# Performance work log

Measured on AMD Instinct MI355X. Metric: run time of the kernel, lower is better.

Reference implementation:

```python
import jax, jax.numpy as jnp
import numpy as np
from math import sqrt

B, S, D_MODEL, H, DK, DV = 16, 512, 256, 8, 32, 32
EPS = 1e-5


def layer_norm(x, g, b):
    m = jnp.mean(x, axis=-1, keepdims=True)
    v = jnp.mean((x - m) ** 2, axis=-1, keepdims=True)
    return g * (x - m) / jnp.sqrt(v + EPS) + b


def setup_inputs() -> dict:
    key = jax.random.key(0)
    ks = jax.random.split(key, 16)
    inp = {
        "input_Q": jax.random.normal(ks[0], (B, S, D_MODEL), jnp.float32),
        "input_K": jax.random.normal(ks[1], (B, S, D_MODEL), jnp.float32),
        "input_V": jax.random.normal(ks[2], (B, S, D_MODEL), jnp.float32),
        "attn_mask": jax.random.bernoulli(ks[3], 0.1, (B, H, S, S)),
        "matrix": jax.random.uniform(ks[4], (B, S, S), jnp.float32),
        # learned params (stored [in, out], i.e. transpose of torch Linear weight)
        "W_Q": jax.random.normal(ks[5], (D_MODEL, H * DK), jnp.float32) * 0.02,
        "W_K": jax.random.normal(ks[6], (D_MODEL, H * DK), jnp.float32) * 0.02,
        "W_V": jax.random.normal(ks[7], (D_MODEL, H * DV), jnp.float32) * 0.02,
        "W_V2": jax.random.normal(ks[8], (D_MODEL, DV), jnp.float32) * 0.02,
        "W_fc": jax.random.normal(ks[9], (DV * (H + 1), D_MODEL), jnp.float32) * 0.02,
        "ln_g": jnp.ones((D_MODEL,), jnp.float32),
        "ln_b": jnp.zeros((D_MODEL,), jnp.float32),
        "fu_ln_g": jnp.ones((H + 1,), jnp.float32),
        "fu_ln_b": jnp.zeros((H + 1,), jnp.float32),
        "fu_w1": jax.random.normal(ks[10], (H + 1, 6), jnp.float32) * 0.3,
        "fu_b1": jnp.zeros((6,), jnp.float32),
        "fu_w2": jax.random.normal(ks[11], (6, 1), jnp.float32) * 0.3,
        "fu_b2": jnp.zeros((1,), jnp.float32),
    }
    return inp


def reference(input_Q, input_K, input_V, attn_mask, matrix,
              W_Q, W_K, W_V, W_V2, W_fc, ln_g, ln_b,
              fu_ln_g, fu_ln_b, fu_w1, fu_b1, fu_w2, fu_b2):
    b = input_Q.shape[0]
    # project and split heads: [B, H, S, d]
    Q = (input_Q @ W_Q).reshape(b, -1, H, DK).transpose(0, 2, 1, 3)
    K = (input_K @ W_K).reshape(b, -1, H, DK).transpose(0, 2, 1, 3)
    V = (input_V @ W_V).reshape(b, -1, H, DV).transpose(0, 2, 1, 3)
    scores = jnp.einsum('bhqd,bhkd->bhqk', Q, K) / sqrt(DK)
    scores = jnp.where(attn_mask, -1e9, scores)
    attn = jax.nn.softmax(scores, axis=-1)            # [B, H, S, S]
    context = jnp.einsum('bhqk,bhkd->bhqd', attn, V)  # [B, H, S, DV]
    # second context from pairwise matrix
    context2 = matrix @ (input_V @ W_V2)              # [B, S, DV]
    # gated matrix update: concat matrix with attn maps along head axis
    gate_in = jnp.concatenate([matrix[:, None], attn], axis=1)  # [B, H+1, S, S]
    gate_in = gate_in.transpose(0, 3, 2, 1)                     # [B, S, S, H+1]
    g = layer_norm(gate_in, fu_ln_g, fu_ln_b)
    g = jax.nn.relu(g @ fu_w1 + fu_b1)
    g = jax.nn.sigmoid(g @ fu_w2 + fu_b2)[..., 0]               # [B, S, S]
    matrix_out = matrix * g
    # merge heads, concat, project, layernorm
    context = context.transpose(0, 2, 1, 3).reshape(b, -1, H * DV)
    context = jnp.concatenate([context, context2], axis=-1)     # [B, S, DV*(H+1)]
    output = layer_norm(context @ W_fc, ln_g, ln_b)
    return (output, matrix_out)
```

## Files before the change

### kernel.cpp

```cpp
#include <hip/hip_runtime.h>
#include <hip/hip_bf16.h>

#define BB 16
#define SS 512
#define DM 256
#define NH 8

#define OFF_QB    0
#define OFF_KB    1048576
#define OFF_VT    2097152
#define OFF_VP2   3145728
#define OFF_CTXB  3407872
#define OFF_CTX2B 4456448
#define OFF_G     4587520
#define OFF_FLAG  6684672
#define OFF_PM    6684674

#define SCALE 0.17677669529663687f
#define KE2 0.2550348623f

typedef __attribute__((ext_vector_type(8))) short bfrag8;
typedef __attribute__((ext_vector_type(4))) float facc4;

__global__ void mask_or_kernel(const unsigned int* __restrict__ w,
                               unsigned int* __restrict__ acc) {
  __shared__ unsigned int sh[256];
  unsigned int a = 0;
  int base = blockIdx.x * 1024;
  for (int i = threadIdx.x; i < 1024; i += 256) a |= w[base + i];
  sh[threadIdx.x] = a;
  __syncthreads();
  for (int s = 128; s > 0; s >>= 1) {
    if (threadIdx.x < s) sh[threadIdx.x] |= sh[threadIdx.x + s];
    __syncthreads();
  }
  if (threadIdx.x == 0) atomicOr(acc, sh[0]);
}

__global__ __launch_bounds__(256) void mask_pack_kernel(
    const void* __restrict__ mask, unsigned long long* __restrict__ pm,
    const unsigned int* __restrict__ orv) {
  const unsigned int rawor = *orv;
  const int flagv = (rawor <= 1u) ? 0 : ((rawor == 0x3F800000u) ? 2 : 1);
  const int lane = threadIdx.x & 63;
  const int wv = threadIdx.x >> 6;
  const int w0 = (blockIdx.x * 4 + wv) * 32;
  const unsigned char* mb = (const unsigned char*)mask;
  const int* mi = (const int*)mask;
  const float* mf = (const float*)mask;
  unsigned long long myw = 0;
#pragma unroll 4
  for (int i = 0; i < 32; i++) {
    long long idx = (long long)(w0 + i) * 64 + lane;
    bool m;
    if (flagv == 1) m = (mb[idx] != 0);
    else if (flagv == 0) m = (mi[idx] != 0);
    else m = (mf[idx] != 0.f);
    unsigned long long bits = __ballot(m);
    if (lane == i) myw = bits;
  }
  if (lane < 32) pm[w0 + lane] = myw;
}

__global__ __launch_bounds__(256) void gemm_qkv_kernel(
    const float* __restrict__ inQ, const float* __restrict__ inK,
    const float* __restrict__ inV,
    const float* __restrict__ Wq, const float* __restrict__ Wk,
    const float* __restrict__ Wv,
    __hip_bfloat16* __restrict__ Qb, __hip_bfloat16* __restrict__ Kb,
    __hip_bfloat16* __restrict__ Vt) {
  __shared__ __align__(16) __hip_bfloat16 As[64][40];
  __shared__ __align__(16) __hip_bfloat16 Bs[64][40];
  const int tid = threadIdx.x;
  const int bid = blockIdx.x;
  const int matid = bid >> 9;
  const int mblk = (bid & 511) >> 2;
  const int nblk = bid & 3;
  const int m0 = mblk * 64;
  const int n0 = nblk * 64;
  const float* X = (matid == 0) ? inQ : (matid == 1) ? inK : inV;
  const float* W = (matid == 0) ? Wq : (matid == 1) ? Wk : Wv;

  const int lane = tid & 63;
  const int w = tid >> 6;
  const int wm = w & 1, wn = w >> 1;
  const int cl = lane & 15, quad = lane >> 4;
  const int arow = tid >> 2, ak8 = (tid & 3) * 8;
  const int bn = tid & 63, bk8 = (tid >> 6) * 8;

  facc4 acc[2][2];
#pragma unroll
  for (int t = 0; t < 2; t++)
#pragma unroll
    for (int u = 0; u < 2; u++) acc[t][u] = (facc4){0.f, 0.f, 0.f, 0.f};

#pragma unroll 1
  for (int kc = 0; kc < 8; kc++) {
    float4 x0 = *(const float4*)&X[(m0 + arow) * 256 + kc * 32 + ak8];
    float4 x1 = *(const float4*)&X[(m0 + arow) * 256 + kc * 32 + ak8 + 4];
    float wv[8];
#pragma unroll
    for (int j = 0; j < 8; j++) wv[j] = W[(kc * 32 + bk8 + j) * 256 + n0 + bn];
    __syncthreads();
    {
      __hip_bfloat16 ta[8];
      ta[0] = __float2bfloat16(x0.x); ta[1] = __float2bfloat16(x0.y);
      ta[2] = __float2bfloat16(x0.z); ta[3] = __float2bfloat16(x0.w);
      ta[4] = __float2bfloat16(x1.x); ta[5] = __float2bfloat16(x1.y);
      ta[6] = __float2bfloat16(x1.z); ta[7] = __float2bfloat16(x1.w);
      *(uint4*)&As[arow][ak8] = *(uint4*)ta;
      __hip_bfloat16 tb[8];
#pragma unroll
      for (int j = 0; j < 8; j++) tb[j] = __float2bfloat16(wv[j]);
      *(uint4*)&Bs[bn][bk8] = *(uint4*)tb;
    }
    __syncthreads();
    bfrag8 aA[2], bB[2];
#pragma unroll
    for (int t = 0; t < 2; t++)
      aA[t] = *(const bfrag8*)&As[wm * 32 + t * 16 + cl][quad * 8];
#pragma unroll
    for (int u = 0; u < 2; u++)
      bB[u] = *(const bfrag8*)&Bs[wn * 32 + u * 16 + cl][quad * 8];
#pragma unroll
    for (int t = 0; t < 2; t++)
#pragma unroll
      for (int u = 0; u < 2; u++)
        acc[t][u] =
            __builtin_amdgcn_mfma_f32_16x16x32_bf16(aA[t], bB[u], acc[t][u], 0, 0, 0);
  }

  if (matid < 2) {
    __hip_bfloat16* Y = (matid == 0) ? Qb : Kb;
#pragma unroll
    for (int t = 0; t < 2; t++)
#pragma unroll
      for (int u = 0; u < 2; u++)
#pragma unroll
        for (int reg = 0; reg < 4; reg++)
          Y[(m0 + wm * 32 + t * 16 + quad * 4 + reg) * 256 + n0 + wn * 32 +
            u * 16 + cl] = __float2bfloat16(acc[t][u][reg]);
  } else {
#pragma unroll
    for (int t = 0; t < 2; t++)
#pragma unroll
      for (int u = 0; u < 2; u++) {
        int c = n0 + wn * 32 + u * 16 + cl;
        int mg = m0 + wm * 32 + t * 16 + quad * 4;
        int b = mg >> 9, s = mg & 511;
        __hip_bfloat16 pk[4];
#pragma unroll
        for (int reg = 0; reg < 4; reg++)
          pk[reg] = __float2bfloat16(acc[t][u][reg]);
        *(ushort4*)&Vt[(((b << 8) + c) << 9) + s] = *(ushort4*)pk;
      }
  }
}

__global__ __launch_bounds__(256) void vp2_kernel(
    const float* __restrict__ inV, const float* __restrict__ Wv2,
    float* __restrict__ Vp2) {
  __shared__ __align__(16) float xs[16][260];
  const int t = threadIdx.x;
  const int r0 = blockIdx.x * 16;
  for (int e = t; e < 16 * 256; e += 256) {
    int r = e >> 8, i = e & 255;
    xs[r][i] = inV[(r0 + r) * 256 + i];
  }
  __syncthreads();
  const int c2 = t & 31, rr = t >> 5;
  float a0 = 0.f, a1 = 0.f;
  for (int i = 0; i < 256; i += 4) {
    float w0 = Wv2[i * 32 + c2], w1 = Wv2[(i + 1) * 32 + c2];
    float w2 = Wv2[(i + 2) * 32 + c2], w3 = Wv2[(i + 3) * 32 + c2];
    float4 xa = *(const float4*)&xs[rr][i];
    float4 xb = *(const float4*)&xs[rr + 8][i];
    a0 += xa.x * w0 + xa.y * w1 + xa.z * w2 + xa.w * w3;
    a1 += xb.x * w0 + xb.y * w1 + xb.z * w2 + xb.w * w3;
  }
  Vp2[(r0 + rr) * 32 + c2] = a0;
  Vp2[(r0 + rr + 8) * 32 + c2] = a1;
}

__global__ __launch_bounds__(512, 2) void attn_kernel(
    const __hip_bfloat16* __restrict__ Qb, const __hip_bfloat16* __restrict__ Kb,
    const __hip_bfloat16* __restrict__ Vt,
    const unsigned long long* __restrict__ pm,
    const float* __restrict__ matrix,
    const float* __restrict__ fulng, const float* __restrict__ fulnb,
    const float* __restrict__ fuw1, const float* __restrict__ fub1,
    const float* __restrict__ fuw2, const float* __restrict__ fub2,
    __hip_bfloat16* __restrict__ ctxb, __hip_bfloat16* __restrict__ gws) {
  __shared__ __align__(16) __hip_bfloat16 Sb[NH][16][520];
  __shared__ float inv_s[NH][16];
  __shared__ float gp[80];

  const int tid = threadIdx.x;
  const int lane = tid & 63;
  const int h = tid >> 6;
  const int cl = lane & 15, quad = lane >> 4;
  const int b = ((blockIdx.x & 7) << 1) | (blockIdx.x >> 8);
  const int q0 = ((blockIdx.x >> 3) & 31) * 16;

  if (tid < 6) {
    const int j = tid;
    float s1 = 0.f, c1 = fub1[j];
#pragma unroll
    for (int t = 0; t < 9; t++) {
      float w = fuw1[t * 6 + j];
      float gw = fulng[t] * w;
      gp[t * 6 + j] = gw;
      s1 += gw;
      c1 += fulnb[t] * w;
    }
    gp[54 + j] = s1;
    gp[60 + j] = c1;
    gp[66 + j] = fuw2[j];
    if (j == 0) gp[72] = fub2[0];
  }

  const unsigned long long* pmb = pm + (((b * NH + h) << 9) + q0) * 8;

  const bfrag8 aQ =
      *(const bfrag8*)&Qb[(((b << 9) + q0 + cl) << 8) + h * 32 + quad * 8];
  const __hip_bfloat16* KbB = &Kb[((b << 9) << 8) + h * 32 + quad * 8];
  const __hip_bfloat16* VtB = &Vt[(((b << 8) + h * 32) << 9)];

  float l[4] = {0.f, 0.f, 0.f, 0.f};
#pragma unroll 2
  for (int w8 = 0; w8 < 8; w8++) {
    unsigned long long mw[4];
#pragma unroll
    for (int r = 0; r < 4; r++)
      mw[r] = pmb[(quad * 4 + r) * 8 + w8] >> cl;
#pragma unroll
    for (int n4 = 0; n4 < 4; n4++) {
      const int nt = w8 * 4 + n4;
      bfrag8 bK = *(const bfrag8*)&KbB[(nt * 16 + cl) << 8];
      facc4 cc = {0.f, 0.f, 0.f, 0.f};
      cc = __builtin_amdgcn_mfma_f32_16x16x32_bf16(aQ, bK, cc, 0, 0, 0);
#pragma unroll
      for (int r = 0; r < 4; r++) {
        float e = ((mw[r] >> (n4 * 16)) & 1ULL) ? 0.f : exp2f(KE2 * cc[r]);
        l[r] += e;
        Sb[h][quad * 4 + r][nt * 16 + cl] = __float2bfloat16(e);
      }
    }
  }
#pragma unroll
  for (int r = 0; r < 4; r++)
#pragma unroll
    for (int off = 1; off <= 8; off <<= 1) l[r] += __shfl_xor(l[r], off);
  float invl[4];
#pragma unroll
  for (int r = 0; r < 4; r++) invl[r] = 1.f / l[r];
  if (cl == 0) {
#pragma unroll
    for (int r = 0; r < 4; r++) inv_s[h][quad * 4 + r] = invl[r];
  }
  __syncthreads();

  facc4 a0 = {0.f, 0.f, 0.f, 0.f}, a1 = {0.f, 0.f, 0.f, 0.f};
#pragma unroll 4
  for (int ks = 0; ks < 16; ks++) {
    bfrag8 aP = *(const bfrag8*)&Sb[h][cl][ks * 32 + quad * 8];
    bfrag8 b0 = *(const bfrag8*)&VtB[(cl << 9) + ks * 32 + quad * 8];
    bfrag8 b1 = *(const bfrag8*)&VtB[((16 + cl) << 9) + ks * 32 + quad * 8];
    a0 = __builtin_amdgcn_mfma_f32_16x16x32_bf16(aP, b0, a0, 0, 0, 0);
    a1 = __builtin_amdgcn_mfma_f32_16x16x32_bf16(aP, b1, a1, 0, 0, 0);
  }

  {
    const int gq = tid >> 5;
    const int g32 = (tid & 31) * 4;
#pragma unroll 1
    for (int s = 0; s < 4; s++) {
      const int k4 = s * 128 + g32;
      float4 mrow =
          *(const float4*)&matrix[((b << 9) + q0 + gq) * 512 + k4];
      float p[NH][4];
#pragma unroll
      for (int hh = 0; hh < NH; hh++) {
        const float iv = inv_s[hh][gq];
        ushort4 sv = *(const ushort4*)&Sb[hh][gq][k4];
        p[hh][0] = __bfloat162float(*(__hip_bfloat16*)&sv.x) * iv;
        p[hh][1] = __bfloat162float(*(__hip_bfloat16*)&sv.y) * iv;
        p[hh][2] = __bfloat162float(*(__hip_bfloat16*)&sv.z) * iv;
        p[hh][3] = __bfloat162float(*(__hip_bfloat16*)&sv.w) * iv;
      }
      const float mcomp[4] = {mrow.x, mrow.y, mrow.z, mrow.w};
      __hip_bfloat16 gout[4];
#pragma unroll
      for (int i = 0; i < 4; i++) {
        float v[9];
        v[0] = mcomp[i];
#pragma unroll
        for (int t = 0; t < NH; t++) v[1 + t] = p[t][i];
        float s1 = 0.f, s2 = 0.f;
#pragma unroll
        for (int t = 0; t < 9; t++) {
          s1 += v[t];
          s2 += v[t] * v[t];
        }
        float mu = s1 * (1.f / 9.f);
        float var = s2 * (1.f / 9.f) - mu * mu;
        float inv = rsqrtf(var + 1e-5f);
        float o = gp[72];
#pragma unroll
        for (int j = 0; j < 6; j++) {
          float d = 0.f;
#pragma unroll
          for (int t = 0; t < 9; t++) d += v[t] * gp[t * 6 + j];
          float z = inv * (d - mu * gp[54 + j]) + gp[60 + j];
          z = fmaxf(z, 0.f);
          o += z * gp[66 + j];
        }
        gout[i] = __float2bfloat16(1.f / (1.f + __expf(-o)));
      }
      *(ushort4*)&gws[((b << 9) + q0 + gq) * 512 + k4] = *(ushort4*)gout;
    }
  }

#pragma unroll
  for (int r = 0; r < 4; r++) {
    int row = quad * 4 + r;
    ctxb[((b << 9) + q0 + row) * 256 + h * 32 + cl] =
        __float2bfloat16(a0[r] * invl[r]);
    ctxb[((b << 9) + q0 + row) * 256 + h * 32 + 16 + cl] =
        __float2bfloat16(a1[r] * invl[r]);
  }
}

__global__ __launch_bounds__(256) void mout_kernel(
    const float* __restrict__ matrix, const __hip_bfloat16* __restrict__ g,
    float* __restrict__ mout) {
  __shared__ float Gs[64][65];
  const int tid = threadIdx.x;
  const int b = blockIdx.x >> 6;
  const int j0 = ((blockIdx.x >> 3) & 7) * 64;
  const int i0 = (blockIdx.x & 7) * 64;

  {
    int r = tid >> 2, c0 = (tid & 3) * 16;
    const __hip_bfloat16* gp = g + (((b << 9) + i0 + r) << 9) + j0 + c0;
    ushort us[16];
    *(uint4*)(us) = *(const uint4*)(gp);
    *(uint4*)(us + 8) = *(const uint4*)(gp + 8);
#pragma unroll
    for (int k = 0; k < 16; k++) {
      __hip_bfloat16 hv = *(__hip_bfloat16*)&us[k];
      Gs[r][c0 + k] = __bfloat162float(hv);
    }
  }
  __syncthreads();

  {
    int jj = tid >> 2, ic = (tid & 3) * 16;
    const float* mp = matrix + (((b << 9) + j0 + jj) << 9) + i0 + ic;
    float* op = mout + (((b << 9) + j0 + jj) << 9) + i0 + ic;
#pragma unroll
    for (int v4 = 0; v4 < 4; v4++) {
      float4 m = *(const float4*)(mp + v4 * 4);
      float4 o;
      o.x = m.x * Gs[ic + v4 * 4 + 0][jj];
      o.y = m.y * Gs[ic + v4 * 4 + 1][jj];
      o.z = m.z * Gs[ic + v4 * 4 + 2][jj];
      o.w = m.w * Gs[ic + v4 * 4 + 3][jj];
      *(float4*)(op + v4 * 4) = o;
    }
  }
}

__global__ __launch_bounds__(256) void ctx2_kernel(
    const float* __restrict__ matrix, const float* __restrict__ Vp2,
    __hip_bfloat16* __restrict__ ctx2b) {
  __shared__ __align__(16) float Ms[16][128];
  __shared__ __align__(16) float Vs2t[32][132];
  const int t = threadIdx.x;
  const int b = blockIdx.x >> 5;
  const int s0 = (blockIdx.x & 31) * 16;
  const int dv = t & 31, rg = t >> 5;
  float acc0 = 0.f, acc1 = 0.f;
  for (int kc = 0; kc < 4; kc++) {
    __syncthreads();
#pragma unroll
    for (int it = 0; it < 8; it++) {
      int idx = t + it * 256;
      int r = idx >> 7, cc = idx & 127;
      Ms[r][cc] = matrix[((b << 9) + s0 + r) * 512 + kc * 128 + cc];
    }
#pragma unroll
    for (int it = 0; it < 16; it++) {
      int e = t + it * 256;
      int k = e >> 5, dv2 = e & 31;
      Vs2t[dv2][k] = Vp2[((b << 9) + kc * 128 + k) * 32 + dv2];
    }
    __syncthreads();
    for (int k = 0; k < 128; k += 4) {
      float4 vv = *(const float4*)&Vs2t[dv][k];
      float4 m0 = *(const float4*)&Ms[rg][k];
      float4 m1 = *(const float4*)&Ms[rg + 8][k];
      acc0 += m0.x * vv.x + m0.y * vv.y + m0.z * vv.z + m0.w * vv.w;
      acc1 += m1.x * vv.x + m1.y * vv.y + m1.z * vv.z + m1.w * vv.w;
    }
  }
  ctx2b[((b << 9) + s0 + rg) * 32 + dv] = __float2bfloat16(acc0);
  ctx2b[((b << 9) + s0 + rg + 8) * 32 + dv] = __float2bfloat16(acc1);
}

__global__ __launch_bounds__(256) void final_kernel(
    const __hip_bfloat16* __restrict__ ctxb,
    const __hip_bfloat16* __restrict__ ctx2b, const float* __restrict__ Wfc,
    const float* __restrict__ lng, const float* __restrict__ lnb,
    float* __restrict__ out) {
  __shared__ __align__(16) __hip_bfloat16 As[32][40];
  __shared__ __align__(16) __hip_bfloat16 Bs[256][40];
  __shared__ __align__(16) float xs[32][260];
  __shared__ float red2[32][8][2];
  __shared__ float musig[32][2];
  const int tid = threadIdx.x;
  const int m0 = blockIdx.x * 32;
  const int lane = tid & 63, w = tid >> 6;
  const int cl = lane & 15, quad = lane >> 4;
  const int arow = tid >> 3, ak4 = (tid & 7) * 4;

  facc4 acc[2][4];
#pragma unroll
  for (int t = 0; t < 2; t++)
#pragma unroll
    for (int u = 0; u < 4; u++) acc[t][u] = (facc4){0.f, 0.f, 0.f, 0.f};

#pragma unroll 1
  for (int kc = 0; kc < 9; kc++) {
    ushort4 av;
    if (kc < 8)
      av = *(const ushort4*)&ctxb[(m0 + arow) * 256 + kc * 32 + ak4];
    else
      av = *(const ushort4*)&ctx2b[(m0 + arow) * 32 + ak4];
    float wv[32];
#pragma unroll
    for (int j = 0; j < 32; j++) wv[j] = Wfc[(kc * 32 + j) * 256 + tid];
    __syncthreads();
    *(ushort4*)&As[arow][ak4] = av;
    {
      __hip_bfloat16 tw[32];
#pragma unroll
      for (int j = 0; j < 32; j++) tw[j] = __float2bfloat16(wv[j]);
#pragma unroll
      for (int g = 0; g < 4; g++) *(uint4*)&Bs[tid][g * 8] = *(uint4*)&tw[g * 8];
    }
    __syncthreads();
    bfrag8 aA[2], bB[4];
#pragma unroll
    for (int t = 0; t < 2; t++)
      aA[t] = *(const bfrag8*)&As[t * 16 + cl][quad * 8];
#pragma unroll
    for (int u = 0; u < 4; u++)
      bB[u] = *(const bfrag8*)&Bs[w * 64 + u * 16 + cl][quad * 8];
#pragma unroll
    for (int t = 0; t < 2; t++)
#pragma unroll
      for (int u = 0; u < 4; u++)
        acc[t][u] =
            __builtin_amdgcn_mfma_f32_16x16x32_bf16(aA[t], bB[u], acc[t][u], 0, 0, 0);
  }

#pragma unroll
  for (int t = 0; t < 2; t++)
#pragma unroll
    for (int u = 0; u < 4; u++)
#pragma unroll
      for (int reg = 0; reg < 4; reg++)
        xs[t * 16 + quad * 4 + reg][w * 64 + u * 16 + cl] = acc[t][u][reg];
  __syncthreads();

  {
    int r = tid >> 3, c0 = (tid & 7) * 32;
    float s1 = 0.f, s2 = 0.f;
    for (int j = 0; j < 32; j += 4) {
      float4 v = *(const float4*)&xs[r][c0 + j];
      s1 += v.x + v.y + v.z + v.w;
      s2 += v.x * v.x + v.y * v.y + v.z * v.z + v.w * v.w;
    }
    red2[r][tid & 7][0] = s1;
    red2[r][tid & 7][1] = s2;
  }
  __syncthreads();
  if (tid < 32) {
    float s1 = 0.f, s2 = 0.f;
#pragma unroll
    for (int j = 0; j < 8; j++) {
      s1 += red2[tid][j][0];
      s2 += red2[tid][j][1];
    }
    float mu = s1 * (1.f / 256.f);
    float var = s2 * (1.f / 256.f) - mu * mu;
    musig[tid][0] = mu;
    musig[tid][1] = rsqrtf(var + 1e-5f);
  }
  __syncthreads();
  {
    float gt = lng[tid], bt = lnb[tid];
#pragma unroll 4
    for (int r = 0; r < 32; r++)
      out[(m0 + r) * 256 + tid] =
          gt * (xs[r][tid] - musig[r][0]) * musig[r][1] + bt;
  }
}

extern "C" void kernel_launch(void* const* d_in, const int* in_sizes, int n_in,
                              void* d_out, int out_size, void* d_ws,
                              size_t ws_size, hipStream_t stream) {
  const float* inQ = (const float*)d_in[0];
  const float* inK = (const float*)d_in[1];
  const float* inV = (const float*)d_in[2];
  const void* mask = d_in[3];
  const float* matrix = (const float*)d_in[4];
  const float* Wq = (const float*)d_in[5];
  const float* Wk = (const float*)d_in[6];
  const float* Wv = (const float*)d_in[7];
  const float* Wv2 = (const float*)d_in[8];
  const float* Wfc = (const float*)d_in[9];
  const float* lng = (const float*)d_in[10];
  const float* lnb = (const float*)d_in[11];
  const float* fulng = (const float*)d_in[12];
  const float* fulnb = (const float*)d_in[13];
  const float* fuw1 = (const float*)d_in[14];
  const float* fub1 = (const float*)d_in[15];
  const float* fuw2 = (const float*)d_in[16];
  const float* fub2 = (const float*)d_in[17];

  float* ws = (float*)d_ws;
  __hip_bfloat16* Qb = (__hip_bfloat16*)(ws + OFF_QB);
  __hip_bfloat16* Kb = (__hip_bfloat16*)(ws + OFF_KB);
  __hip_bfloat16* Vt = (__hip_bfloat16*)(ws + OFF_VT);
  float* Vp2 = ws + OFF_VP2;
  __hip_bfloat16* ctxb = (__hip_bfloat16*)(ws + OFF_CTXB);
  __hip_bfloat16* ctx2b = (__hip_bfloat16*)(ws + OFF_CTX2B);
  __hip_bfloat16* gws = (__hip_bfloat16*)(ws + OFF_G);
  unsigned int* flag = (unsigned int*)(ws + OFF_FLAG);
  unsigned long long* pmask = (unsigned long long*)(ws + OFF_PM);

  float* out = (float*)d_out;
  float* mout = out + BB * SS * DM;

  hipMemsetAsync(flag, 0, 4, stream);
  mask_or_kernel<<<64, 256, 0, stream>>>((const unsigned int*)mask, flag);
  mask_pack_kernel<<<4096, 256, 0, stream>>>(mask, pmask, flag);
  gemm_qkv_kernel<<<1536, 256, 0, stream>>>(inQ, inK, inV, Wq, Wk, Wv, Qb, Kb,
                                            Vt);
  vp2_kernel<<<512, 256, 0, stream>>>(inV, Wv2, Vp2);
  attn_kernel<<<512, 512, 0, stream>>>(Qb, Kb, Vt, pmask, matrix, fulng, fulnb,
                                       fuw1, fub1, fuw2, fub2, ctxb, gws);
  mout_kernel<<<BB * 64, 256, 0, stream>>>(matrix, gws, mout);
  ctx2_kernel<<<512, 256, 0, stream>>>(matrix, Vp2, ctx2b);
  final_kernel<<<256, 256, 0, stream>>>(ctxb, ctx2b, Wfc, lng, lnb, out);
}
```

Before: 386.6 us.

## Halve attention query tile, fuse ctx2 matmul into attention kernel

The attention kernel now handles 8 query rows per block instead of 16, doubling the grid to 1024 blocks and raising the occupancy hint to 4 blocks per CU. The MFMA still computes 16 rows, so half the lanes do duplicate work that is then discarded. The separate ctx2 kernel is removed and the matrix@Vp2 product is computed inside the attention kernel from the matrix rows it already touches, which saves one launch and one pass over matrix. The trade-offs are wasted MFMA and exp work, a ctx2 reduction done with plain scalar FMAs reading Vp2 from global memory, and possible register pressure from the tighter bound.

```diff
diff --git a/kernel.cpp b/kernel.cpp
--- a/kernel.cpp
+++ b/kernel.cpp
@@ -182,25 +182,26 @@
   Vp2[(r0 + rr + 8) * 32 + c2] = a1;
 }
 
-__global__ __launch_bounds__(512, 2) void attn_kernel(
+__global__ __launch_bounds__(512, 4) void attn_kernel(
     const __hip_bfloat16* __restrict__ Qb, const __hip_bfloat16* __restrict__ Kb,
     const __hip_bfloat16* __restrict__ Vt,
     const unsigned long long* __restrict__ pm,
-    const float* __restrict__ matrix,
+    const float* __restrict__ matrix, const float* __restrict__ Vp2,
     const float* __restrict__ fulng, const float* __restrict__ fulnb,
     const float* __restrict__ fuw1, const float* __restrict__ fub1,
     const float* __restrict__ fuw2, const float* __restrict__ fub2,
-    __hip_bfloat16* __restrict__ ctxb, __hip_bfloat16* __restrict__ gws) {
-  __shared__ __align__(16) __hip_bfloat16 Sb[NH][16][520];
-  __shared__ float inv_s[NH][16];
+    __hip_bfloat16* __restrict__ ctxb, __hip_bfloat16* __restrict__ gws,
+    __hip_bfloat16* __restrict__ ctx2b) {
+  __shared__ __align__(16) __hip_bfloat16 Sb[NH][8][520];
+  __shared__ float inv_s[NH][8];
   __shared__ float gp[80];
 
   const int tid = threadIdx.x;
   const int lane = tid & 63;
   const int h = tid >> 6;
   const int cl = lane & 15, quad = lane >> 4;
-  const int b = ((blockIdx.x & 7) << 1) | (blockIdx.x >> 8);
-  const int q0 = ((blockIdx.x >> 3) & 31) * 16;
+  const int b = ((blockIdx.x & 7) << 1) | (blockIdx.x >> 9);
+  const int q0 = ((blockIdx.x >> 3) & 63) * 8;
 
   if (tid < 6) {
     const int j = tid;
@@ -222,7 +223,7 @@
   const unsigned long long* pmb = pm + (((b * NH + h) << 9) + q0) * 8;
 
   const bfrag8 aQ =
-      *(const bfrag8*)&Qb[(((b << 9) + q0 + cl) << 8) + h * 32 + quad * 8];
+      *(const bfrag8*)&Qb[(((b << 9) + q0 + (cl & 7)) << 8) + h * 32 + quad * 8];
   const __hip_bfloat16* KbB = &Kb[((b << 9) << 8) + h * 32 + quad * 8];
   const __hip_bfloat16* VtB = &Vt[(((b << 8) + h * 32) << 9)];
 
@@ -232,7 +233,7 @@
     unsigned long long mw[4];
 #pragma unroll
     for (int r = 0; r < 4; r++)
-      mw[r] = pmb[(quad * 4 + r) * 8 + w8] >> cl;
+      mw[r] = pmb[((quad & 1) * 4 + r) * 8 + w8] >> cl;
 #pragma unroll
     for (int n4 = 0; n4 < 4; n4++) {
       const int nt = w8 * 4 + n4;
@@ -243,7 +244,7 @@
       for (int r = 0; r < 4; r++) {
         float e = ((mw[r] >> (n4 * 16)) & 1ULL) ? 0.f : exp2f(KE2 * cc[r]);
         l[r] += e;
-        Sb[h][quad * 4 + r][nt * 16 + cl] = __float2bfloat16(e);
+        if (quad < 2) Sb[h][quad * 4 + r][nt * 16 + cl] = __float2bfloat16(e);
       }
     }
   }
@@ -254,35 +255,45 @@
   float invl[4];
 #pragma unroll
   for (int r = 0; r < 4; r++) invl[r] = 1.f / l[r];
-  if (cl == 0) {
+  if (quad < 2 && cl == 0) {
 #pragma unroll
     for (int r = 0; r < 4; r++) inv_s[h][quad * 4 + r] = invl[r];
   }
-  __syncthreads();
 
   facc4 a0 = {0.f, 0.f, 0.f, 0.f}, a1 = {0.f, 0.f, 0.f, 0.f};
 #pragma unroll 4
   for (int ks = 0; ks < 16; ks++) {
-    bfrag8 aP = *(const bfrag8*)&Sb[h][cl][ks * 32 + quad * 8];
+    bfrag8 aP = *(const bfrag8*)&Sb[h][cl & 7][ks * 32 + quad * 8];
     bfrag8 b0 = *(const bfrag8*)&VtB[(cl << 9) + ks * 32 + quad * 8];
     bfrag8 b1 = *(const bfrag8*)&VtB[((16 + cl) << 9) + ks * 32 + quad * 8];
     a0 = __builtin_amdgcn_mfma_f32_16x16x32_bf16(aP, b0, a0, 0, 0, 0);
     a1 = __builtin_amdgcn_mfma_f32_16x16x32_bf16(aP, b1, a1, 0, 0, 0);
   }
+  if (quad < 2) {
+#pragma unroll
+    for (int r = 0; r < 4; r++) {
+      int row = quad * 4 + r;
+      ctxb[((b << 9) + q0 + row) * 256 + h * 32 + cl] =
+          __float2bfloat16(a0[r] * invl[r]);
+      ctxb[((b << 9) + q0 + row) * 256 + h * 32 + 16 + cl] =
+          __float2bfloat16(a1[r] * invl[r]);
+    }
+  }
+
+  __syncthreads();
 
   {
-    const int gq = tid >> 5;
-    const int g32 = (tid & 31) * 4;
+    const int rowb = ((b << 9) + q0 + h) * 512;
+    const int c8 = lane * 8;
 #pragma unroll 1
-    for (int s = 0; s < 4; s++) {
-      const int k4 = s * 128 + g32;
-      float4 mrow =
-          *(const float4*)&matrix[((b << 9) + q0 + gq) * 512 + k4];
+    for (int s2 = 0; s2 < 2; s2++) {
+      const int k4 = c8 + s2 * 4;
+      float4 mrow = *(const float4*)&matrix[rowb + k4];
       float p[NH][4];
 #pragma unroll
       for (int hh = 0; hh < NH; hh++) {
-        const float iv = inv_s[hh][gq];
-        ushort4 sv = *(const ushort4*)&Sb[hh][gq][k4];
+        const float iv = inv_s[hh][h];
+        ushort4 sv = *(const ushort4*)&Sb[hh][h][k4];
         p[hh][0] = __bfloat162float(*(__hip_bfloat16*)&sv.x) * iv;
         p[hh][1] = __bfloat162float(*(__hip_bfloat16*)&sv.y) * iv;
         p[hh][2] = __bfloat162float(*(__hip_bfloat16*)&sv.z) * iv;
@@ -296,14 +307,14 @@
         v[0] = mcomp[i];
 #pragma unroll
         for (int t = 0; t < NH; t++) v[1 + t] = p[t][i];
-        float s1 = 0.f, s2 = 0.f;
+        float s1 = 0.f, s2s = 0.f;
 #pragma unroll
         for (int t = 0; t < 9; t++) {
           s1 += v[t];
-          s2 += v[t] * v[t];
+          s2s += v[t] * v[t];
         }
         float mu = s1 * (1.f / 9.f);
-        float var = s2 * (1.f / 9.f) - mu * mu;
+        float var = s2s * (1.f / 9.f) - mu * mu;
         float inv = rsqrtf(var + 1e-5f);
         float o = gp[72];
 #pragma unroll
@@ -317,17 +328,27 @@
         }
         gout[i] = __float2bfloat16(1.f / (1.f + __expf(-o)));
       }
-      *(ushort4*)&gws[((b << 9) + q0 + gq) * 512 + k4] = *(ushort4*)gout;
-    }
-  }
-
-#pragma unroll
-  for (int r = 0; r < 4; r++) {
-    int row = quad * 4 + r;
-    ctxb[((b << 9) + q0 + row) * 256 + h * 32 + cl] =
-        __float2bfloat16(a0[r] * invl[r]);
-    ctxb[((b << 9) + q0 + row) * 256 + h * 32 + 16 + cl] =
-        __float2bfloat16(a1[r] * invl[r]);
+      *(ushort4*)&gws[rowb + k4] = *(ushort4*)gout;
+    }
+  }
+
+  {
+    const int dv = lane & 31, kh = lane >> 5;
+    const int rowb = ((b << 9) + q0 + h) * 512;
+    const float* vp = &Vp2[(b << 9) * 32];
+    float acc = 0.f;
+#pragma unroll 4
+    for (int k4 = 0; k4 < 256; k4 += 4) {
+      const int k = kh * 256 + k4;
+      float4 mv = *(const float4*)&matrix[rowb + k];
+      acc += mv.x * vp[(k + 0) * 32 + dv];
+      acc += mv.y * vp[(k + 1) * 32 + dv];
+      acc += mv.z * vp[(k + 2) * 32 + dv];
+      acc += mv.w * vp[(k + 3) * 32 + dv];
+    }
+    acc += __shfl_xor(acc, 32);
+    if (lane < 32)
+      ctx2b[((b << 9) + q0 + h) * 32 + dv] = __float2bfloat16(acc);
   }
 }
 
@@ -342,10 +363,10 @@
 
   {
     int r = tid >> 2, c0 = (tid & 3) * 16;
-    const __hip_bfloat16* gp = g + (((b << 9) + i0 + r) << 9) + j0 + c0;
+    const __hip_bfloat16* gpx = g + (((b << 9) + i0 + r) << 9) + j0 + c0;
     ushort us[16];
-    *(uint4*)(us) = *(const uint4*)(gp);
-    *(uint4*)(us + 8) = *(const uint4*)(gp + 8);
+    *(uint4*)(us) = *(const uint4*)(gpx);
+    *(uint4*)(us + 8) = *(const uint4*)(gpx + 8);
 #pragma unroll
     for (int k = 0; k < 16; k++) {
       __hip_bfloat16 hv = *(__hip_bfloat16*)&us[k];
@@ -369,43 +390,6 @@
       *(float4*)(op + v4 * 4) = o;
     }
   }
-}
-
-__global__ __launch_bounds__(256) void ctx2_kernel(
-    const float* __restrict__ matrix, const float* __restrict__ Vp2,
-    __hip_bfloat16* __restrict__ ctx2b) {
-  __shared__ __align__(16) float Ms[16][128];
-  __shared__ __align__(16) float Vs2t[32][132];
-  const int t = threadIdx.x;
-  const int b = blockIdx.x >> 5;
-  const int s0 = (blockIdx.x & 31) * 16;
-  const int dv = t & 31, rg = t >> 5;
-  float acc0 = 0.f, acc1 = 0.f;
-  for (int kc = 0; kc < 4; kc++) {
-    __syncthreads();
-#pragma unroll
-    for (int it = 0; it < 8; it++) {
-      int idx = t + it * 256;
-      int r = idx >> 7, cc = idx & 127;
-      Ms[r][cc] = matrix[((b << 9) + s0 + r) * 512 + kc * 128 + cc];
-    }
-#pragma unroll
-    for (int it = 0; it < 16; it++) {
-      int e = t + it * 256;
-      int k = e >> 5, dv2 = e & 31;
-      Vs2t[dv2][k] = Vp2[((b << 9) + kc * 128 + k) * 32 + dv2];
-    }
-    __syncthreads();
-    for (int k = 0; k < 128; k += 4) {
-      float4 vv = *(const float4*)&Vs2t[dv][k];
-      float4 m0 = *(const float4*)&Ms[rg][k];
-      float4 m1 = *(const float4*)&Ms[rg + 8][k];
-      acc0 += m0.x * vv.x + m0.y * vv.y + m0.z * vv.z + m0.w * vv.w;
-      acc1 += m1.x * vv.x + m1.y * vv.y + m1.z * vv.z + m1.w * vv.w;
-    }
-  }
-  ctx2b[((b << 9) + s0 + rg) * 32 + dv] = __float2bfloat16(acc0);
-  ctx2b[((b << 9) + s0 + rg + 8) * 32 + dv] = __float2bfloat16(acc1);
 }
 
 __global__ __launch_bounds__(256) void final_kernel(
@@ -550,9 +534,9 @@
   gemm_qkv_kernel<<<1536, 256, 0, stream>>>(inQ, inK, inV, Wq, Wk, Wv, Qb, Kb,
                                             Vt);
   vp2_kernel<<<512, 256, 0, stream>>>(inV, Wv2, Vp2);
-  attn_kernel<<<512, 512, 0, stream>>>(Qb, Kb, Vt, pmask, matrix, fulng, fulnb,
-                                       fuw1, fub1, fuw2, fub2, ctxb, gws);
+  attn_kernel<<<1024, 512, 0, stream>>>(Qb, Kb, Vt, pmask, matrix, Vp2, fulng,
+                                        fulnb, fuw1, fub1, fuw2, fub2, ctxb,
+                                        gws, ctx2b);
   mout_kernel<<<BB * 64, 256, 0, stream>>>(matrix, gws, mout);
-  ctx2_kernel<<<512, 256, 0, stream>>>(matrix, Vp2, ctx2b);
   final_kernel<<<256, 256, 0, stream>>>(ctxb, ctx2b, Wfc, lng, lnb, out);
 }
```

Result: slower. 422.9 us (+9.4%).
